# Performance work log

Hardware: AMD Instinct MI355X
Metric: run time of the kernel (lower is better)

Reference implementation:

```python
import jax, jax.numpy as jnp
import numpy as np

HIDDEN = 512
NHEADS = 8
ALPHA = 0.1
NUM_HOP = 4
MASK_VAL = -16384.0
LN_EPS = 1e-5


def setup_inputs() -> dict:
    key = jax.random.key(0)
    ks = jax.random.split(key, 10)
    B, N, H = 8, 1024, HIDDEN
    s = 1.0 / np.sqrt(H)
    x = jax.random.normal(ks[0], (B, N, H), dtype=jnp.float32)
    adj = jax.random.randint(ks[1], (B, N, N), 0, 2, dtype=jnp.int32)
    Wq = jax.random.uniform(ks[2], (H, H), jnp.float32, -s, s)
    bq = jax.random.uniform(ks[3], (H,), jnp.float32, -s, s)
    Wk = jax.random.uniform(ks[4], (H, H), jnp.float32, -s, s)
    bk = jax.random.uniform(ks[5], (H,), jnp.float32, -s, s)
    Wv = jax.random.uniform(ks[6], (H, H), jnp.float32, -s, s)
    bv = jax.random.uniform(ks[7], (H,), jnp.float32, -s, s)
    gamma = jnp.ones((H,), jnp.float32)
    beta = jnp.zeros((H,), jnp.float32)
    return {"x": x, "adj": adj, "Wq": Wq, "bq": bq, "Wk": Wk, "bk": bk,
            "Wv": Wv, "bv": bv, "gamma": gamma, "beta": beta}


def reference(x, adj, Wq, bq, Wk, bk, Wv, bv, gamma, beta):
    B, N, H = x.shape
    u = H // NHEADS
    # torch Linear: y = x @ W^T + b
    q = x @ Wq.T + bq  # [B,N,H]
    k = x @ Wk.T + bk
    v = x @ Wv.T + bv
    # split hidden into contiguous head chunks (matches per-head slicing)
    qh = q.reshape(B, N, NHEADS, u).transpose(0, 2, 1, 3)  # [B,Hd,N,u]
    kh = k.reshape(B, N, NHEADS, u).transpose(0, 2, 1, 3)
    vh = v.reshape(B, N, NHEADS, u).transpose(0, 2, 1, 3)
    scores = jnp.einsum('bhnd,bhmd->bhnm', qh, kh)  # [B,Hd,N,N]
    mask = (adj == 0)[:, None, :, :]  # broadcast over heads
    scores = jnp.where(mask, MASK_VAL, scores)
    pros = jax.nn.softmax(scores, axis=-1)
    z_init = vh
    z = z_init
    for _ in range(NUM_HOP):
        z = (1.0 - ALPHA) * jnp.einsum('bhnm,bhmd->bhnd', pros, z) + ALPHA * z_init
    h_prime = z.transpose(0, 2, 1, 3).reshape(B, N, H)  # concat heads
    y = x + h_prime
    mu = jnp.mean(y, axis=-1, keepdims=True)
    var = jnp.mean((y - mu) ** 2, axis=-1, keepdims=True)
    return (y - mu) / jnp.sqrt(var + LN_EPS) * gamma + beta
```

## Files before the change

### kernel.cpp

```cpp
#include <hip/hip_runtime.h>
#include <hip/hip_bf16.h>

#define BB 8
#define NN 1024
#define HH 512
#define NHEADS 8
#define UU 64

typedef __attribute__((ext_vector_type(8))) short short8;
typedef __attribute__((ext_vector_type(4))) float f32x4;
typedef unsigned short u16;
typedef unsigned char u8;

__device__ inline float b2f(unsigned short u) {
    union { float f; unsigned int i; } c; c.i = ((unsigned int)u) << 16; return c.f;
}
__device__ inline unsigned short f2b(float f) {
    __hip_bfloat16 h = __float2bfloat16(f);
    return *reinterpret_cast<unsigned short*>(&h);
}
__device__ inline void gl_lds16(const void* g, void* l) {
    __builtin_amdgcn_global_load_lds(
        (const __attribute__((address_space(1))) unsigned int*)g,
        (__attribute__((address_space(3))) unsigned int*)l, 16, 0, 0);
}

__global__ __launch_bounds__(256) void cvt_w(
    const float* __restrict__ Wq, const float* __restrict__ Wk,
    const float* __restrict__ Wv, u16* __restrict__ Wb)
{
    const int which = blockIdx.y;
    const float* src = which == 0 ? Wq : (which == 1 ? Wk : Wv);
    u16* dst = Wb + (size_t)which * HH * HH;
    const int base = (blockIdx.x * 256 + threadIdx.x) * 8;
    const float4* sp = (const float4*)&src[base];
    float4 a = sp[0], b = sp[1];
    short8 o;
    o[0] = (short)f2b(a.x); o[1] = (short)f2b(a.y);
    o[2] = (short)f2b(a.z); o[3] = (short)f2b(a.w);
    o[4] = (short)f2b(b.x); o[5] = (short)f2b(b.y);
    o[6] = (short)f2b(b.z); o[7] = (short)f2b(b.w);
    *(short8*)&dst[base] = o;
}

__global__ __launch_bounds__(256) void adj_pack(
    const int* __restrict__ adj, unsigned int* __restrict__ adjp)
{
    const int wave = threadIdx.x >> 6, lane = threadIdx.x & 63;
    const int row = blockIdx.x * 4 + wave;
    const int* ar = adj + (size_t)row * NN;
    unsigned long long* out = (unsigned long long*)(adjp + (size_t)row * 32);
    #pragma unroll
    for (int it = 0; it < 16; ++it) {
        int a = ar[it * 64 + lane];
        unsigned long long m = __ballot(a != 0);
        if (lane == 0) out[it] = m;
    }
}

__global__ __launch_bounds__(256) void qkv_gemm(
    const float* __restrict__ x, const u16* __restrict__ Wb,
    const float* __restrict__ bq, const float* __restrict__ bk,
    const float* __restrict__ bv,
    u16* __restrict__ q, u16* __restrict__ k, u16* __restrict__ v)
{
    const int which = blockIdx.z;
    const u16* W      = Wb + (size_t)which * HH * HH;
    const float* bias = which == 0 ? bq : (which == 1 ? bk : bv);
    u16* out          = which == 0 ? q  : (which == 1 ? k  : v);

    const int tid = threadIdx.x;
    const int wave = tid >> 6, lane = tid & 63;
    const int ln = lane & 15, quad = lane >> 4;
    const int wr = (wave >> 1) * 64, wc = (wave & 1) * 64;
    const int rowbase = blockIdx.x * 128, colbase = blockIdx.y * 128;

    __shared__ __align__(16) u16 As[128 * 40];
    __shared__ __align__(16) u16 Bs[128 * 32];
    __shared__ __align__(16) u16 Cs[128 * 136];

    f32x4 acc[4][4];
    #pragma unroll
    for (int ri = 0; ri < 4; ++ri)
        #pragma unroll
        for (int ci = 0; ci < 4; ++ci) acc[ri][ci] = (f32x4){0.f, 0.f, 0.f, 0.f};

    const int lr = lane >> 2;
    const int sg = lane & 3;

    for (int kk = 0; kk < HH; kk += 32) {
        __syncthreads();
        #pragma unroll
        for (int i = 0; i < 2; ++i) {
            int r = wave * 32 + i * 16 + lr;
            const float* xp = &x[(size_t)(rowbase + r) * HH + kk + sg * 8];
            float4 f0 = *(const float4*)xp, f1 = *(const float4*)(xp + 4);
            short8 o;
            o[0] = (short)f2b(f0.x); o[1] = (short)f2b(f0.y);
            o[2] = (short)f2b(f0.z); o[3] = (short)f2b(f0.w);
            o[4] = (short)f2b(f1.x); o[5] = (short)f2b(f1.y);
            o[6] = (short)f2b(f1.z); o[7] = (short)f2b(f1.w);
            *(short8*)&As[r * 40 + sg * 8] = o;
            gl_lds16(&W[(size_t)(colbase + r) * HH + kk + sg * 8],
                     (char*)Bs + (wave * 32 + i * 16) * 64);
        }
        __syncthreads();

        short8 bfr[4];
        #pragma unroll
        for (int ci = 0; ci < 4; ++ci)
            bfr[ci] = *(const short8*)&Bs[(wc + ci * 16 + ln) * 32 + quad * 8];
        #pragma unroll
        for (int ri = 0; ri < 4; ++ri) {
            short8 af = *(const short8*)&As[(wr + ri * 16 + ln) * 40 + quad * 8];
            #pragma unroll
            for (int ci = 0; ci < 4; ++ci)
                acc[ri][ci] = __builtin_amdgcn_mfma_f32_16x16x32_bf16(af, bfr[ci], acc[ri][ci], 0, 0, 0);
        }
    }

    #pragma unroll
    for (int ci = 0; ci < 4; ++ci) {
        int col = wc + ci * 16 + ln;
        float bb = bias[colbase + col];
        #pragma unroll
        for (int ri = 0; ri < 4; ++ri) {
            #pragma unroll
            for (int r = 0; r < 4; ++r) {
                int row = wr + ri * 16 + quad * 4 + r;
                Cs[row * 136 + col] = f2b(acc[ri][ci][r] + bb);
            }
        }
    }
    __syncthreads();
    {
        int row = tid >> 1, half = tid & 1;
        int gcol0 = colbase + half * 64;
        int hh = gcol0 >> 6;
        int grow = rowbase + row;
        int bidx = grow >> 10, n = grow & 1023;
        u16* op = &out[(((size_t)(bidx * NHEADS + hh)) * NN + n) * UU];
        const u16* cp = &Cs[row * 136 + half * 64];
        #pragma unroll
        for (int j = 0; j < 8; ++j)
            *(short8*)(op + j * 8) = *(const short8*)(cp + j * 8);
    }
}

__global__ __launch_bounds__(256) void vt8(
    const u16* __restrict__ v, u8* __restrict__ v8t)
{
    const int bh = blockIdx.x >> 2, part = blockIdx.x & 3;
    const int t = threadIdx.x;
    const size_t hd = (size_t)bh << 16;
    __shared__ u16 tile[64][72];

    for (int chunk = part * 4; chunk < part * 4 + 4; ++chunk) {
        const int n0 = chunk * 64;
        const int r = t >> 2, cs = t & 3;
        const u16* vp = &v[((size_t)bh * NN + n0 + r) * UU + cs * 16];
        short8 a = *(const short8*)vp;
        short8 b8 = *(const short8*)(vp + 8);
        #pragma unroll
        for (int j = 0; j < 8; ++j) {
            tile[r][cs * 16 + j] = (u16)a[j];
            tile[r][cs * 16 + 8 + j] = (u16)b8[j];
        }
        __syncthreads();
        const int c = t & 63, qt = t >> 6;
        unsigned int w[4];
        #pragma unroll
        for (int g = 0; g < 4; ++g) {
            float f0 = b2f(tile[qt * 16 + g * 4 + 0][c]);
            float f1 = b2f(tile[qt * 16 + g * 4 + 1][c]);
            float f2 = b2f(tile[qt * 16 + g * 4 + 2][c]);
            float f3 = b2f(tile[qt * 16 + g * 4 + 3][c]);
            int lo = __builtin_amdgcn_cvt_pk_fp8_f32(f0, f1, 0, false);
            w[g] = (unsigned int)__builtin_amdgcn_cvt_pk_fp8_f32(f2, f3, lo, true);
        }
        uint4 o; o.x = w[0]; o.y = w[1]; o.z = w[2]; o.w = w[3];
        *(uint4*)&v8t[hd + (size_t)c * 1024 + n0 + qt * 16] = o;
        __syncthreads();
    }
}

__global__ __launch_bounds__(256) void scores_softmax(
    const u16* __restrict__ q, const u16* __restrict__ kmat,
    const unsigned int* __restrict__ adjp, u8* __restrict__ P8)
{
    const int b = blockIdx.z, h = blockIdx.y, rt = blockIdx.x;
    const int bh = b * NHEADS + h;
    const int tid = threadIdx.x;
    const int wave = tid >> 6, lane = tid & 63;
    const int ln = lane & 15, quad = lane >> 4;
    const int wrow = rt * 64 + wave * 16;

    __shared__ __align__(16) u16 ks[128 * 72];
    __shared__ __align__(16) u16 eb[64 * 136];

    const u16* qp = &q[((size_t)bh * NN + wrow + ln) * UU + quad * 8];
    short8 a0 = *(const short8*)qp;
    short8 a1 = *(const short8*)(qp + 32);

    float rsum[4] = {0.f, 0.f, 0.f, 0.f};
    float scl[4];

    const int srow = tid >> 3;
    const int sseg = tid & 7;

    for (int pass = 0; pass < 2; ++pass) {
        for (int cc = 0; cc < 8; ++cc) {
            __syncthreads();
            #pragma unroll
            for (int j = 0; j < 4; ++j) {
                int kr = j * 32 + srow;
                uint4 kv = *(const uint4*)&kmat[((size_t)bh * NN + cc * 128 + kr) * UU + sseg * 8];
                *(uint4*)&ks[kr * 72 + sseg * 8] = kv;
            }
            __syncthreads();

            unsigned int ab[4][4];
            #pragma unroll
            for (int r = 0; r < 4; ++r) {
                int row = wrow + quad * 4 + r;
                *(uint4*)&ab[r][0] =
                    *(const uint4*)&adjp[((size_t)(b * NN + row)) * 32 + cc * 4];
            }

            #pragma unroll
            for (int ct = 0; ct < 8; ++ct) {
                const u16* kp = &ks[(ct * 16 + ln) * 72 + quad * 8];
                short8 b0 = *(const short8*)kp;
                short8 b1 = *(const short8*)(kp + 32);
                f32x4 acc = (f32x4){0.f, 0.f, 0.f, 0.f};
                acc = __builtin_amdgcn_mfma_f32_16x16x32_bf16(a0, b0, acc, 0, 0, 0);
                acc = __builtin_amdgcn_mfma_f32_16x16x32_bf16(a1, b1, acc, 0, 0, 0);
                const int dw = ct >> 1;
                const int bitpos = (ct & 1) * 16 + ln;
                #pragma unroll
                for (int r = 0; r < 4; ++r) {
                    unsigned int on = (ab[r][dw] >> bitpos) & 1u;
                    float e = on ? __expf(acc[r] - 32.0f) : 0.0f;
                    if (pass == 0) rsum[r] += e;
                    else eb[(wave * 16 + quad * 4 + r) * 136 + ct * 16 + ln] = f2b(e * scl[r]);
                }
            }

            if (pass == 1) {
                const int kcp = lane >> 4, r16 = lane & 15;
                const u16* ep = &eb[(wave * 16 + r16) * 136 + kcp * 32];
                unsigned int w[8];
                #pragma unroll
                for (int g2 = 0; g2 < 4; ++g2) {
                    short8 ev = *(const short8*)(ep + g2 * 8);
                    float f0 = b2f((u16)ev[0]);
                    float f1 = b2f((u16)ev[1]);
                    float f2 = b2f((u16)ev[2]);
                    float f3 = b2f((u16)ev[3]);
                    int lo = __builtin_amdgcn_cvt_pk_fp8_f32(f0, f1, 0, false);
                    w[g2 * 2] = (unsigned int)__builtin_amdgcn_cvt_pk_fp8_f32(f2, f3, lo, true);
                    f0 = b2f((u16)ev[4]);
                    f1 = b2f((u16)ev[5]);
                    f2 = b2f((u16)ev[6]);
                    f3 = b2f((u16)ev[7]);
                    lo = __builtin_amdgcn_cvt_pk_fp8_f32(f0, f1, 0, false);
                    w[g2 * 2 + 1] = (unsigned int)__builtin_amdgcn_cvt_pk_fp8_f32(f2, f3, lo, true);
                }
                u8* op = P8 + ((size_t)bh << 20) + (size_t)(rt * 4 + wave) * 16384
                       + (cc * 4 + kcp) * 512 + r16 * 32;
                uint4 o0; o0.x = w[0]; o0.y = w[1]; o0.z = w[2]; o0.w = w[3];
                uint4 o1; o1.x = w[4]; o1.y = w[5]; o1.z = w[6]; o1.w = w[7];
                *(uint4*)op = o0;
                *(uint4*)(op + 16) = o1;
            }
        }
        if (pass == 0) {
            #pragma unroll
            for (int r = 0; r < 4; ++r) {
                #pragma unroll
                for (int off = 8; off >= 1; off >>= 1)
                    rsum[r] += __shfl_xor(rsum[r], off);
                scl[r] = 16.0f / rsum[r];
            }
        }
    }
}

__global__ __launch_bounds__(512) void hop(
    const u8* __restrict__ P8, const u8* __restrict__ z8in,
    const u16* __restrict__ v, u8* __restrict__ z8out,
    u16* __restrict__ zbf_out, int last)
{
    const int b = blockIdx.z, h = blockIdx.y, rt = blockIdx.x;
    const int bh = b * NHEADS + h;
    const int tid = threadIdx.x;
    const int wave = tid >> 6, lane = tid & 63;
    const int ln = lane & 15, quad = lane >> 4;
    const int wrow = rt * 128 + wave * 16;

    __shared__ __align__(16) u8 zt[64 * 1040];

    const u8* zg = z8in + ((size_t)bh << 16);
    #pragma unroll
    for (int i = 0; i < 8; ++i) {
        int c = wave * 8 + i;
        gl_lds16(zg + (size_t)c * 1024 + lane * 16, (char*)zt + c * 1040);
    }
    __syncthreads();

    f32x4 acc[4];
    #pragma unroll
    for (int ci = 0; ci < 4; ++ci) acc[ci] = (f32x4){0.f, 0.f, 0.f, 0.f};

    const u8* pt = P8 + ((size_t)bh << 20) + (size_t)(rt * 8 + wave) * 16384
                 + ln * 32 + quad * 8;
    #pragma unroll 4
    for (int kc = 0; kc < 32; ++kc) {
        long a = *(const long*)(pt + kc * 512);
        int kk = kc * 32;
        #pragma unroll
        for (int ci = 0; ci < 4; ++ci) {
            long bz = *(const long*)&zt[(ci * 16 + ln) * 1040 + kk + quad * 8];
            acc[ci] = __builtin_amdgcn_mfma_f32_16x16x32_fp8_fp8(a, bz, acc[ci], 0, 0, 0);
        }
    }

    if (last) {
        #pragma unroll
        for (int ci = 0; ci < 4; ++ci) {
            int col = ci * 16 + ln;
            #pragma unroll
            for (int r = 0; r < 4; ++r) {
                int row = wrow + quad * 4 + r;
                float vv = b2f(v[((size_t)bh * NN + row) * UU + col]);
                zbf_out[((size_t)(b * NN + row)) * HH + h * UU + col]
                    = f2b(0.05625f * acc[ci][r] + 0.1f * vv);
            }
        }
    } else {
        u8* zo = z8out + ((size_t)bh << 16);
        #pragma unroll
        for (int ci = 0; ci < 4; ++ci) {
            int col = ci * 16 + ln;
            float zv[4];
            #pragma unroll
            for (int r = 0; r < 4; ++r) {
                int row = wrow + quad * 4 + r;
                float vv = b2f(v[((size_t)bh * NN + row) * UU + col]);
                zv[r] = 0.05625f * acc[ci][r] + 0.1f * vv;
            }
            int lo = __builtin_amdgcn_cvt_pk_fp8_f32(zv[0], zv[1], 0, false);
            unsigned int dw = (unsigned int)__builtin_amdgcn_cvt_pk_fp8_f32(zv[2], zv[3], lo, true);
            *(unsigned int*)&zo[(size_t)col * 1024 + wrow + quad * 4] = dw;
        }
    }
}

__global__ __launch_bounds__(256) void resid_ln(
    const float* __restrict__ x, const u16* __restrict__ z,
    const float* __restrict__ gamma, const float* __restrict__ beta,
    float* __restrict__ out)
{
    const int r = blockIdx.x * 4 + (threadIdx.x >> 6);
    const int lane = threadIdx.x & 63;
    const size_t base = (size_t)r * HH + lane * 8;

    const float4* xp = (const float4*)&x[base];
    float4 x0 = xp[0], x1 = xp[1];
    short8 zv = *(const short8*)&z[base];
    float y[8];
    y[0] = x0.x + b2f((u16)zv[0]); y[1] = x0.y + b2f((u16)zv[1]);
    y[2] = x0.z + b2f((u16)zv[2]); y[3] = x0.w + b2f((u16)zv[3]);
    y[4] = x1.x + b2f((u16)zv[4]); y[5] = x1.y + b2f((u16)zv[5]);
    y[6] = x1.z + b2f((u16)zv[6]); y[7] = x1.w + b2f((u16)zv[7]);

    float s = 0.f, sq = 0.f;
    #pragma unroll
    for (int j = 0; j < 8; ++j) { s += y[j]; sq += y[j] * y[j]; }
    #pragma unroll
    for (int off = 32; off >= 1; off >>= 1) {
        s  += __shfl_xor(s, off);
        sq += __shfl_xor(sq, off);
    }
    const float mu = s * (1.0f / HH);
    const float var = sq * (1.0f / HH) - mu * mu;
    const float rstd = rsqrtf(var + 1e-5f);

    const float4* gp = (const float4*)&gamma[lane * 8];
    const float4* bp = (const float4*)&beta[lane * 8];
    float4 g0 = gp[0], g1 = gp[1], b0 = bp[0], b1 = bp[1];

    float4 o0, o1;
    o0.x = (y[0] - mu) * rstd * g0.x + b0.x;
    o0.y = (y[1] - mu) * rstd * g0.y + b0.y;
    o0.z = (y[2] - mu) * rstd * g0.z + b0.z;
    o0.w = (y[3] - mu) * rstd * g0.w + b0.w;
    o1.x = (y[4] - mu) * rstd * g1.x + b1.x;
    o1.y = (y[5] - mu) * rstd * g1.y + b1.y;
    o1.z = (y[6] - mu) * rstd * g1.z + b1.z;
    o1.w = (y[7] - mu) * rstd * g1.w + b1.w;
    float4* op = (float4*)&out[base];
    op[0] = o0; op[1] = o1;
}

extern "C" void kernel_launch(void* const* d_in, const int* in_sizes, int n_in,
                              void* d_out, int out_size, void* d_ws, size_t ws_size,
                              hipStream_t stream)
{
    const float* x   = (const float*)d_in[0];
    const int* adj   = (const int*)d_in[1];
    const float* Wq  = (const float*)d_in[2];
    const float* bq  = (const float*)d_in[3];
    const float* Wk  = (const float*)d_in[4];
    const float* bk  = (const float*)d_in[5];
    const float* Wv  = (const float*)d_in[6];
    const float* bv  = (const float*)d_in[7];
    const float* gamma = (const float*)d_in[8];
    const float* beta  = (const float*)d_in[9];
    float* out = (float*)d_out;

    const size_t E = (size_t)BB * NN * HH;
    u16* ws16 = (u16*)d_ws;
    u16* q  = ws16 + E;
    u16* k  = ws16 + 2 * E;
    u16* v  = ws16 + 3 * E;
    u16* za = ws16 + 4 * E;
    u16* Wb = ws16 + 5 * E;
    u8* base8 = (u8*)(ws16 + 5 * E + 786432);
    u8* P8  = base8;
    u8* z8a = base8 + ((size_t)64 << 20);
    u8* z8b = z8a + ((size_t)4 << 20);
    u8* v8t = z8b + ((size_t)4 << 20);
    unsigned int* adjp = (unsigned int*)(v8t + ((size_t)4 << 20));

    cvt_w<<<dim3(128, 3), 256, 0, stream>>>(Wq, Wk, Wv, Wb);
    adj_pack<<<dim3(2048), 256, 0, stream>>>(adj, adjp);
    qkv_gemm<<<dim3(64, 4, 3), 256, 0, stream>>>(x, Wb, bq, bk, bv, q, k, v);
    vt8<<<dim3(256), 256, 0, stream>>>(v, v8t);
    scores_softmax<<<dim3(16, NHEADS, BB), 256, 0, stream>>>(q, k, adjp, P8);
    hop<<<dim3(8, NHEADS, BB), 512, 0, stream>>>(P8, v8t, v, z8a, za, 0);
    hop<<<dim3(8, NHEADS, BB), 512, 0, stream>>>(P8, z8a, v, z8b, za, 0);
    hop<<<dim3(8, NHEADS, BB), 512, 0, stream>>>(P8, z8b, v, z8a, za, 0);
    hop<<<dim3(8, NHEADS, BB), 512, 0, stream>>>(P8, z8a, v, z8b, za, 1);
    resid_ln<<<dim3(2048), 256, 0, stream>>>(x, za, gamma, beta, out);
}
```

Baseline: 287.9 us.

## Rewrite scores_softmax with 32x32 MFMA, transposed adjacency bitmask and direct FP8 stores

```diff
diff --git a/kernel.cpp b/kernel.cpp
--- a/kernel.cpp
+++ b/kernel.cpp
@@ -9,6 +9,7 @@
 
 typedef __attribute__((ext_vector_type(8))) short short8;
 typedef __attribute__((ext_vector_type(4))) float f32x4;
+typedef __attribute__((ext_vector_type(16))) float f32x16;
 typedef unsigned short u16;
 typedef unsigned char u8;
 
@@ -44,17 +45,21 @@
 }
 
 __global__ __launch_bounds__(256) void adj_pack(
-    const int* __restrict__ adj, unsigned int* __restrict__ adjp)
+    const int* __restrict__ adj, unsigned int* __restrict__ adjpT)
 {
     const int wave = threadIdx.x >> 6, lane = threadIdx.x & 63;
     const int row = blockIdx.x * 4 + wave;
+    const int b = row >> 10, r = row & 1023;
     const int* ar = adj + (size_t)row * NN;
-    unsigned long long* out = (unsigned long long*)(adjp + (size_t)row * 32);
+    unsigned int* ob = adjpT + (((size_t)b) << 15) + r;
     #pragma unroll
     for (int it = 0; it < 16; ++it) {
         int a = ar[it * 64 + lane];
         unsigned long long m = __ballot(a != 0);
-        if (lane == 0) out[it] = m;
+        if (lane == 0) {
+            ob[(size_t)(2 * it)     << 10] = (unsigned int)m;
+            ob[(size_t)(2 * it + 1) << 10] = (unsigned int)(m >> 32);
+        }
     }
 }
 
@@ -184,104 +189,78 @@
     }
 }
 
+__device__ inline f32x16 score_tile(const u16* kp, unsigned int m2,
+                                    const short8* qf)
+{
+    short8 kf[4];
+    #pragma unroll
+    for (int f = 0; f < 4; ++f) kf[f] = *(const short8*)(kp + f * 16);
+    f32x16 acc;
+    #pragma unroll
+    for (int j = 0; j < 16; ++j) {
+        const int koff = (j & 3) + 8 * (j >> 2);
+        acc[j] = ((m2 >> koff) & 1u) ? -32.0f : -16384.0f;
+    }
+    #pragma unroll
+    for (int f = 0; f < 4; ++f)
+        acc = __builtin_amdgcn_mfma_f32_32x32x16_bf16(kf[f], qf[f], acc, 0, 0, 0);
+    return acc;
+}
+
 __global__ __launch_bounds__(256) void scores_softmax(
     const u16* __restrict__ q, const u16* __restrict__ kmat,
-    const unsigned int* __restrict__ adjp, u8* __restrict__ P8)
-{
-    const int b = blockIdx.z, h = blockIdx.y, rt = blockIdx.x;
+    const unsigned int* __restrict__ adjpT, u8* __restrict__ P8)
+{
+    const int b = blockIdx.z, h = blockIdx.y;
     const int bh = b * NHEADS + h;
     const int tid = threadIdx.x;
     const int wave = tid >> 6, lane = tid & 63;
-    const int ln = lane & 15, quad = lane >> 4;
-    const int wrow = rt * 64 + wave * 16;
-
-    __shared__ __align__(16) u16 ks[128 * 72];
-    __shared__ __align__(16) u16 eb[64 * 136];
-
-    const u16* qp = &q[((size_t)bh * NN + wrow + ln) * UU + quad * 8];
-    short8 a0 = *(const short8*)qp;
-    short8 a1 = *(const short8*)(qp + 32);
-
-    float rsum[4] = {0.f, 0.f, 0.f, 0.f};
-    float scl[4];
-
-    const int srow = tid >> 3;
-    const int sseg = tid & 7;
-
-    for (int pass = 0; pass < 2; ++pass) {
-        for (int cc = 0; cc < 8; ++cc) {
-            __syncthreads();
-            #pragma unroll
-            for (int j = 0; j < 4; ++j) {
-                int kr = j * 32 + srow;
-                uint4 kv = *(const uint4*)&kmat[((size_t)bh * NN + cc * 128 + kr) * UU + sseg * 8];
-                *(uint4*)&ks[kr * 72 + sseg * 8] = kv;
-            }
-            __syncthreads();
-
-            unsigned int ab[4][4];
-            #pragma unroll
-            for (int r = 0; r < 4; ++r) {
-                int row = wrow + quad * 4 + r;
-                *(uint4*)&ab[r][0] =
-                    *(const uint4*)&adjp[((size_t)(b * NN + row)) * 32 + cc * 4];
-            }
-
-            #pragma unroll
-            for (int ct = 0; ct < 8; ++ct) {
-                const u16* kp = &ks[(ct * 16 + ln) * 72 + quad * 8];
-                short8 b0 = *(const short8*)kp;
-                short8 b1 = *(const short8*)(kp + 32);
-                f32x4 acc = (f32x4){0.f, 0.f, 0.f, 0.f};
-                acc = __builtin_amdgcn_mfma_f32_16x16x32_bf16(a0, b0, acc, 0, 0, 0);
-                acc = __builtin_amdgcn_mfma_f32_16x16x32_bf16(a1, b1, acc, 0, 0, 0);
-                const int dw = ct >> 1;
-                const int bitpos = (ct & 1) * 16 + ln;
-                #pragma unroll
-                for (int r = 0; r < 4; ++r) {
-                    unsigned int on = (ab[r][dw] >> bitpos) & 1u;
-                    float e = on ? __expf(acc[r] - 32.0f) : 0.0f;
-                    if (pass == 0) rsum[r] += e;
-                    else eb[(wave * 16 + quad * 4 + r) * 136 + ct * 16 + ln] = f2b(e * scl[r]);
-                }
-            }
-
-            if (pass == 1) {
-                const int kcp = lane >> 4, r16 = lane & 15;
-                const u16* ep = &eb[(wave * 16 + r16) * 136 + kcp * 32];
-                unsigned int w[8];
-                #pragma unroll
-                for (int g2 = 0; g2 < 4; ++g2) {
-                    short8 ev = *(const short8*)(ep + g2 * 8);
-                    float f0 = b2f((u16)ev[0]);
-                    float f1 = b2f((u16)ev[1]);
-                    float f2 = b2f((u16)ev[2]);
-                    float f3 = b2f((u16)ev[3]);
-                    int lo = __builtin_amdgcn_cvt_pk_fp8_f32(f0, f1, 0, false);
-                    w[g2 * 2] = (unsigned int)__builtin_amdgcn_cvt_pk_fp8_f32(f2, f3, lo, true);
-                    f0 = b2f((u16)ev[4]);
-                    f1 = b2f((u16)ev[5]);
-                    f2 = b2f((u16)ev[6]);
-                    f3 = b2f((u16)ev[7]);
-                    lo = __builtin_amdgcn_cvt_pk_fp8_f32(f0, f1, 0, false);
-                    w[g2 * 2 + 1] = (unsigned int)__builtin_amdgcn_cvt_pk_fp8_f32(f2, f3, lo, true);
-                }
-                u8* op = P8 + ((size_t)bh << 20) + (size_t)(rt * 4 + wave) * 16384
-                       + (cc * 4 + kcp) * 512 + r16 * 32;
-                uint4 o0; o0.x = w[0]; o0.y = w[1]; o0.z = w[2]; o0.w = w[3];
-                uint4 o1; o1.x = w[4]; o1.y = w[5]; o1.z = w[6]; o1.w = w[7];
-                *(uint4*)op = o0;
-                *(uint4*)(op + 16) = o1;
-            }
-        }
-        if (pass == 0) {
-            #pragma unroll
-            for (int r = 0; r < 4; ++r) {
-                #pragma unroll
-                for (int off = 8; off >= 1; off >>= 1)
-                    rsum[r] += __shfl_xor(rsum[r], off);
-                scl[r] = 16.0f / rsum[r];
-            }
+    const int l31 = lane & 31, hi = lane >> 5;
+    const int rg = wave >> 1, kh = wave & 1;
+    const int n = (blockIdx.x * 2 + rg) * 32 + l31;
+    const int kt0 = kh * 16, kt1 = kt0 + 16;
+
+    __shared__ float rs[2][2][32];
+
+    short8 qf[4];
+    const u16* qp = &q[((size_t)bh * NN + n) * UU + hi * 8];
+    #pragma unroll
+    for (int f = 0; f < 4; ++f) qf[f] = *(const short8*)(qp + f * 16);
+
+    const u16* kbase = kmat + (size_t)bh * NN * UU + hi * 8;
+    const unsigned int* mbase = adjpT + (((size_t)b) << 15) + n;
+
+    float rsum = 0.f;
+    #pragma unroll 2
+    for (int t = kt0; t < kt1; ++t) {
+        const unsigned int m2 = mbase[(size_t)t << 10] >> (4 * hi);
+        const u16* kp = kbase + (size_t)(t * 32 + l31) * UU;
+        f32x16 acc = score_tile(kp, m2, qf);
+        #pragma unroll
+        for (int j = 0; j < 16; ++j) rsum += __expf(acc[j]);
+    }
+    rsum += __shfl_xor(rsum, 32);
+    if (lane < 32) rs[rg][kh][lane] = rsum;
+    __syncthreads();
+    const float scl = 16.0f / (rs[rg][0][l31] + rs[rg][1][l31]);
+
+    u8* pb = P8 + (((size_t)bh) << 20) + (size_t)(n >> 4) * 16384
+           + (n & 15) * 32 + hi * 4;
+    #pragma unroll 2
+    for (int t = kt0; t < kt1; ++t) {
+        const unsigned int m2 = mbase[(size_t)t << 10] >> (4 * hi);
+        const u16* kp = kbase + (size_t)(t * 32 + l31) * UU;
+        f32x16 acc = score_tile(kp, m2, qf);
+        u8* pt = pb + (size_t)t * 512;
+        #pragma unroll
+        for (int g = 0; g < 4; ++g) {
+            float e0 = __expf(acc[g * 4 + 0]) * scl;
+            float e1 = __expf(acc[g * 4 + 1]) * scl;
+            float e2 = __expf(acc[g * 4 + 2]) * scl;
+            float e3 = __expf(acc[g * 4 + 3]) * scl;
+            int lo = __builtin_amdgcn_cvt_pk_fp8_f32(e0, e1, 0, false);
+            unsigned int dw = (unsigned int)__builtin_amdgcn_cvt_pk_fp8_f32(e2, e3, lo, true);
+            *(unsigned int*)(pt + g * 8) = dw;
         }
     }
 }
@@ -431,13 +410,13 @@
     u8* z8a = base8 + ((size_t)64 << 20);
     u8* z8b = z8a + ((size_t)4 << 20);
     u8* v8t = z8b + ((size_t)4 << 20);
-    unsigned int* adjp = (unsigned int*)(v8t + ((size_t)4 << 20));
+    unsigned int* adjpT = (unsigned int*)(v8t + ((size_t)4 << 20));
 
     cvt_w<<<dim3(128, 3), 256, 0, stream>>>(Wq, Wk, Wv, Wb);
-    adj_pack<<<dim3(2048), 256, 0, stream>>>(adj, adjp);
+    adj_pack<<<dim3(2048), 256, 0, stream>>>(adj, adjpT);
     qkv_gemm<<<dim3(64, 4, 3), 256, 0, stream>>>(x, Wb, bq, bk, bv, q, k, v);
     vt8<<<dim3(256), 256, 0, stream>>>(v, v8t);
-    scores_softmax<<<dim3(16, NHEADS, BB), 256, 0, stream>>>(q, k, adjp, P8);
+    scores_softmax<<<dim3(16, NHEADS, BB), 256, 0, stream>>>(q, k, adjpT, P8);
     hop<<<dim3(8, NHEADS, BB), 512, 0, stream>>>(P8, v8t, v, z8a, za, 0);
     hop<<<dim3(8, NHEADS, BB), 512, 0, stream>>>(P8, z8a, v, z8b, za, 0);
     hop<<<dim3(8, NHEADS, BB), 512, 0, stream>>>(P8, z8b, v, z8a, za, 0);
```

After: 301.0 us. 1.05x slower.
